# Kernel tuning notes

Measured on AMD Instinct MI355X. Metric: run time of the kernel, lower is better.

Reference implementation:

```python
import jax, jax.numpy as jnp
import numpy as np

THETA = 10000.0


def apply_rope(x, token_position, theta=THETA):
    # x: [B, H, S, d_k] with interleaved even/odd pairs; token_position: [B, S]
    B, H, S, d_k = x.shape
    inv_freq = 1.0 / theta ** (jnp.arange(0, d_k, 2, dtype=jnp.float32) / d_k)  # [d_k/2]
    angles = token_position.astype(jnp.float32)[:, :, None] * inv_freq[None, None, :]  # [B,S,d_k/2]
    cos = jnp.cos(angles)[:, None, :, :]  # [B,1,S,d_k/2]
    sin = jnp.sin(angles)[:, None, :, :]
    xp = x.reshape(B, H, S, d_k // 2, 2)
    x_even, x_odd = xp[..., 0], xp[..., 1]
    rot_even = x_even * cos - x_odd * sin
    rot_odd = x_even * sin + x_odd * cos
    return jnp.stack([rot_even, rot_odd], axis=-1).reshape(B, H, S, d_k)


def setup_inputs() -> dict:
    key = jax.random.key(0)
    ks = jax.random.split(key, 6)
    B, S, D = 2, 2048, 2048
    x = jax.random.normal(ks[0], (B, S, D), dtype=jnp.float32)
    token_position = jnp.sort(jax.random.randint(ks[1], (B, S), 0, 2048), axis=-1).astype(jnp.int32)
    scale = 0.02
    WQ = jax.random.normal(ks[2], (D, D), dtype=jnp.float32) * scale
    WK = jax.random.normal(ks[3], (D, D), dtype=jnp.float32) * scale
    WV = jax.random.normal(ks[4], (D, D), dtype=jnp.float32) * scale
    WO = jax.random.normal(ks[5], (D, D), dtype=jnp.float32) * scale
    return {"x": x, "token_position": token_position, "WQ": WQ, "WK": WK, "WV": WV, "WO": WO}


def reference(x, token_position, WQ, WK, WV, WO):
    B, S, D = x.shape
    H = 16
    d_k = D // H

    def proj(W):
        return jnp.matmul(x, W).reshape(B, S, H, d_k).transpose(0, 2, 1, 3)  # [B,H,S,d_k]

    Q = apply_rope(proj(WQ), token_position)
    K = apply_rope(proj(WK), token_position)
    V = proj(WV)

    score = jnp.einsum('bhqd,bhkd->bhqk', Q, K) / jnp.sqrt(jnp.float32(d_k))
    causal = jnp.triu(jnp.full((S, S), -jnp.inf, dtype=jnp.float32), k=1)
    score = score + causal
    attn = jax.nn.softmax(score, axis=-1)  # stable max-sub softmax, same math
    out = jnp.einsum('bhqk,bhkd->bhqd', attn, V)
    out = out.transpose(0, 2, 1, 3).reshape(B, S, D)
    return jnp.matmul(out, WO)
```

## Files before the change

### kernel.cpp

```cpp
#include <hip/hip_runtime.h>
#include <hip/hip_bf16.h>
#include <cstdint>
#include <cstddef>

typedef unsigned short u16;
typedef __attribute__((ext_vector_type(4))) unsigned short u16x4;
typedef __attribute__((ext_vector_type(8))) unsigned short u16x8;
typedef __attribute__((ext_vector_type(8))) __bf16 bf16x8;
typedef __attribute__((ext_vector_type(4))) float f32x4;

#define MFMA16(a, b, c) __builtin_amdgcn_mfma_f32_16x16x32_bf16((a), (b), (c), 0, 0, 0)

__device__ __forceinline__ u16 f2bf(float f) {
  uint32_t u = __builtin_bit_cast(uint32_t, f);
  u += 0x7FFFu + ((u >> 16) & 1u);
  return (u16)(u >> 16);
}
__device__ __forceinline__ float bf2f(u16 h) {
  return __builtin_bit_cast(float, (uint32_t)h << 16);
}

typedef const __attribute__((address_space(1))) void gv_t;
typedef __attribute__((address_space(3))) void lv_t;
__device__ __forceinline__ void gload16(const void* g, void* l) {
  __builtin_amdgcn_global_load_lds((gv_t*)g, (lv_t*)l, 16, 0, 0);
}

__global__ void prep(const float* __restrict__ x, const float* __restrict__ w0,
                     const float* __restrict__ w1, const float* __restrict__ w2,
                     const float* __restrict__ w3, u16* __restrict__ xb,
                     u16* __restrict__ wtbase) {
  const int z = blockIdx.z;
  const int bx = blockIdx.x, by = blockIdx.y;
  const int tx = threadIdx.x, ty = threadIdx.y;
  if (z >= 4) {
    const int i = ((z - 4) * 4096 + by * 64 + bx) * 256 + ty * 32 + tx;
    float4 v = ((const float4*)x)[i];
    u16x4 o;
    o[0] = f2bf(v.x); o[1] = f2bf(v.y); o[2] = f2bf(v.z); o[3] = f2bf(v.w);
    ((u16x4*)xb)[i] = o;
    return;
  }
  __shared__ float tile[32][33];
  const float* in = (z == 0) ? w0 : (z == 1) ? w1 : (z == 2) ? w2 : w3;
  u16* out = wtbase + (size_t)z * 4194304;
#pragma unroll
  for (int i = 0; i < 32; i += 8)
    tile[ty + i][tx] = in[(size_t)(by * 32 + ty + i) * 2048 + bx * 32 + tx];
  __syncthreads();
#pragma unroll
  for (int i = 0; i < 32; i += 8)
    out[(size_t)(bx * 32 + ty + i) * 2048 + by * 32 + tx] = f2bf(tile[tx][ty + i]);
}

template <int MODE>
__global__ __launch_bounds__(512, 1) void gemm8(const u16* __restrict__ A,
                                                const u16* __restrict__ Bt,
                                                void* __restrict__ Cv,
                                                const int* __restrict__ pos, int nbn) {
  constexpr int K = 2048;
  __shared__ __align__(16) u16 lds[73728];
  const int tid = threadIdx.x, lane = tid & 63;
  const int lo16 = lane & 15, hi = lane >> 4;
  const int wid = tid >> 6;
  const int wr = wid >> 1, wc = wid & 1;

  const int xcd = (int)blockIdx.x & 7;
  const int idx = (int)blockIdx.x >> 3;
  const int cpx = nbn >> 3;
  const int bn = (xcd * cpx + idx % cpx) * 128;
  const int bm = (idx / cpx) * 256;

  const int srow = tid >> 3;
  const int scol = ((tid & 7) ^ (srow & 7)) * 8;
  const u16* Arow = A + (size_t)(bm + srow) * K + scol;
  const u16* Brow = Bt + (size_t)(bn + srow) * K + scol;
  char* dstbase = (char*)lds + tid * 16;

#define STG_A(qb_, t_, r_) \
  gload16(Arow + (size_t)(r_) * 64 * K + (t_) * 64, dstbase + (qb_) * 49152 + (r_) * 8192)
#define STG_B(qb_, t_, r_) \
  gload16(Brow + (size_t)(r_) * 64 * K + (t_) * 64, dstbase + (qb_) * 49152 + 32768 + (r_) * 8192)

  f32x4 acc[4][4];
  const f32x4 z4 = {0.f, 0.f, 0.f, 0.f};
#pragma unroll
  for (int m = 0; m < 4; ++m)
#pragma unroll
    for (int n = 0; n < 4; ++n) acc[m][n] = z4;

  const int xork = lo16 & 7;
  const int aRow = (wr * 64 + lo16) * 128;
  const int bRow = 32768 + (wc * 64 + lo16) * 128;
  const int x0 = ((hi ^ xork)) << 4;
  const int x1 = (((4 + hi) ^ xork)) << 4;

  STG_A(0, 0, 0); STG_A(0, 0, 1); STG_A(0, 0, 2); STG_A(0, 0, 3);
  STG_B(0, 0, 0); STG_B(0, 0, 1);
  STG_A(1, 1, 0); STG_A(1, 1, 1); STG_A(1, 1, 2); STG_A(1, 1, 3);
  STG_B(1, 1, 0); STG_B(1, 1, 1);

  int q = 0;
  for (int t = 0; t < 32; ++t) {
    if (t < 31) {
      asm volatile("s_waitcnt vmcnt(6)" ::: "memory");
    } else {
      asm volatile("s_waitcnt vmcnt(0)" ::: "memory");
    }
    __builtin_amdgcn_s_barrier();
    __builtin_amdgcn_sched_barrier(0);
    const char* Aq = (const char*)lds + q * 49152;
    const int q2 = (q == 0) ? 2 : q - 1;

    bf16x8 a0[4], b0[4], a1[4], b1[4];
#pragma unroll
    for (int m = 0; m < 4; ++m) a0[m] = *(const bf16x8*)(Aq + aRow + m * 2048 + x0);
#pragma unroll
    for (int n = 0; n < 4; ++n) b0[n] = *(const bf16x8*)(Aq + bRow + n * 2048 + x0);
#pragma unroll
    for (int m = 0; m < 4; ++m) a1[m] = *(const bf16x8*)(Aq + aRow + m * 2048 + x1);
#pragma unroll
    for (int n = 0; n < 4; ++n) b1[n] = *(const bf16x8*)(Aq + bRow + n * 2048 + x1);

    if (t < 30) {
      STG_A(q2, t + 2, 0); STG_A(q2, t + 2, 1); STG_A(q2, t + 2, 2); STG_A(q2, t + 2, 3);
      STG_B(q2, t + 2, 0); STG_B(q2, t + 2, 1);
    }

    __builtin_amdgcn_s_setprio(1);
#pragma unroll
    for (int m = 0; m < 4; ++m)
#pragma unroll
      for (int n = 0; n < 4; ++n) acc[m][n] = MFMA16(a0[m], b0[n], acc[m][n]);
#pragma unroll
    for (int m = 0; m < 4; ++m)
#pragma unroll
      for (int n = 0; n < 4; ++n) acc[m][n] = MFMA16(a1[m], b1[n], acc[m][n]);
    __builtin_amdgcn_s_setprio(0);
    q = (q == 2) ? 0 : q + 1;
  }
#undef STG_A
#undef STG_B

  if constexpr (MODE == 2) {
    const int sect = bn >> 11;
    u16* Cq = (u16*)Cv + (size_t)sect * 8388608;
    const int cb = (bn & 2047) + wc * 64;
    if (sect < 2) {
      const float qsc = (sect == 0) ? 0.12751743f : 1.0f;
      float freq[4];
#pragma unroll
      for (int n = 0; n < 4; ++n) {
        const int c = cb + n * 16 + lo16;
        freq[n] = exp2f((float)((c & 127) >> 1) * -0.2076205059304601f);
      }
      const float sg = (lo16 & 1) ? 1.f : -1.f;
#pragma unroll
      for (int m = 0; m < 4; ++m) {
        const int row = bm + wr * 64 + m * 16 + hi * 4;
#pragma unroll
        for (int r = 0; r < 4; ++r) {
          const float p = (float)pos[row + r];
#pragma unroll
          for (int n = 0; n < 4; ++n) {
            const float ang = p * freq[n];
            const float sn = __sinf(ang);
            const float cs = __cosf(ang);
            const float v = acc[m][n][r];
            const float pv = __shfl_xor(v, 1);
            Cq[(size_t)(row + r) * 2048 + cb + n * 16 + lo16] =
                f2bf((v * cs + sg * pv * sn) * qsc);
          }
        }
      }
    } else {
      __syncthreads();
#pragma unroll
      for (int m = 0; m < 4; ++m) {
#pragma unroll
        for (int n = 0; n < 4; ++n) {
          const int d = wc * 64 + n * 16 + lo16;
          const int tokb = wr * 64 + m * 16 + hi * 4;
#pragma unroll
          for (int r = 0; r < 4; ++r)
            lds[d * 260 + tokb + r] = f2bf(acc[m][n][r]);
        }
      }
      __syncthreads();
      const int b = bm >> 11, hh = (bn & 2047) >> 7;
      u16* vt = Cq + ((size_t)((b * 16 + hh) * 128)) * 2048 + (bm & 2047);
#pragma unroll
      for (int j = 0; j < 4; ++j) {
        const int d = (tid >> 4) + j * 32;
        const int t0 = (tid & 15) * 16;
        const u16* src = lds + d * 260 + t0;
        u16* dst = vt + (size_t)d * 2048 + t0;
#pragma unroll
        for (int w = 0; w < 4; ++w)
          *(u16x4*)(dst + w * 4) = *(const u16x4*)(src + w * 4);
      }
    }
  } else {
    float* C = (float*)Cv;
    const int cb = bn + wc * 64;
#pragma unroll
    for (int m = 0; m < 4; ++m)
#pragma unroll
      for (int n = 0; n < 4; ++n)
#pragma unroll
        for (int r = 0; r < 4; ++r)
          C[(size_t)(bm + wr * 64 + m * 16 + hi * 4 + r) * 2048 + cb + n * 16 + lo16] =
              acc[m][n][r];
  }
}

__device__ __forceinline__ void sm_write(f32x4* accS, float* m_r, float* l_r,
                                         f32x4* accO, char* Pw, int lane) {
  float lm[4];
#pragma unroll
  for (int j = 0; j < 4; ++j)
    lm[j] = fmaxf(fmaxf(accS[0][j], accS[1][j]), fmaxf(accS[2][j], accS[3][j]));
  const bool ok = (lm[0] <= m_r[0] + 11.5f) && (lm[1] <= m_r[1] + 11.5f) &&
                  (lm[2] <= m_r[2] + 11.5f) && (lm[3] <= m_r[3] + 11.5f);
  if (!__all(ok)) {
#pragma unroll
    for (int j = 0; j < 4; ++j) {
      float mx = lm[j];
#pragma unroll
      for (int off = 1; off < 16; off <<= 1) mx = fmaxf(mx, __shfl_xor(mx, off));
      const float mn = fmaxf(m_r[j], mx);
      const float sc = exp2f(m_r[j] - mn);
      m_r[j] = mn;
      l_r[j] *= sc;
#pragma unroll
      for (int db = 0; db < 8; ++db) accO[db][j] *= sc;
    }
  }
#pragma unroll
  for (int j = 0; j < 4; ++j) {
    float s = 0.f;
    const int ql = (lane >> 4) * 4 + j;
#pragma unroll
    for (int nb = 0; nb < 4; ++nb) {
      const float p = exp2f(accS[nb][j] - m_r[j]);
      s += p;
      const int col = nb * 16 + (lane & 15);
      const int byteoff = ql * 128 + ((((col >> 3) ^ (ql & 7))) << 4) + (col & 7) * 2;
      *(u16*)(Pw + byteoff) = (u16)(__builtin_bit_cast(uint32_t, p) >> 16);
    }
    l_r[j] += s;
  }
}

__global__ __launch_bounds__(256, 2) void flash_attn9(const u16* __restrict__ Qb,
                                                      const u16* __restrict__ Kb,
                                                      const u16* __restrict__ VT,
                                                      u16* __restrict__ Ob) {
  constexpr int S = 2048, HD = 2048;
  const int g = (int)blockIdx.x;
  const int xcd = g & 7, slot = g >> 3;
  const int bh = xcd * 4 + (slot & 3);
  const int pairid = slot >> 2;
  const int b = bh >> 4, h = bh & 15;
  const int tid = threadIdx.x, lane = tid & 63, wid = tid >> 6;
  const int qtA = 31 - pairid, qtB = pairid;
  const int q0a = qtA * 64, q0b = qtB * 64;

  __shared__ u16 Ks[2][64 * 128];
  __shared__ u16 Vs[2][128 * 64];
  __shared__ u16 Ps[4][2][16 * 64];

  const size_t base = (size_t)b * S * HD + (size_t)h * 128;
  const u16* Qp = Qb + base;
  const u16* Kp = Kb + base;
  const u16* VTp = VT + (size_t)bh * 128 * S;
  u16* Op = Ob + base;

  const f32x4 z4 = {0.f, 0.f, 0.f, 0.f};
  const int kKv = (lane >> 4);
  const int kC16 = (lane & 15);
  const int vD = (lane >> 3);
  const int vC16 = (lane & 7);

#define STAGE(pb, kv0_)                                                                   \
  {                                                                                       \
    _Pragma("unroll") for (int c = 0; c < 4; ++c) {                                       \
      const int ch = wid * 4 + c;                                                         \
      {                                                                                   \
        const int kv = ch * 4 + kKv;                                                      \
        const int c16 = kC16 ^ (kv & 7);                                                  \
        gload16(Kp + (size_t)((kv0_) + kv) * HD + c16 * 8, (char*)Ks[pb] + ch * 1024);    \
      }                                                                                   \
      {                                                                                   \
        const int d = ch * 8 + vD;                                                        \
        const int c16 = vC16 ^ (d & 7);                                                   \
        gload16(VTp + (size_t)d * S + (kv0_) + c16 * 8, (char*)Vs[pb] + ch * 1024);       \
      }                                                                                   \
    }                                                                                     \
  }

  bf16x8 qfA[4], qfB[4];
  {
    const int kc = (lane >> 4) * 8;
    const int qrA = q0a + wid * 16 + (lane & 15);
    const int qrB = q0b + wid * 16 + (lane & 15);
#pragma unroll
    for (int kb = 0; kb < 4; ++kb) {
      qfA[kb] = *(const bf16x8*)(Qp + (size_t)qrA * HD + kb * 32 + kc);
      qfB[kb] = *(const bf16x8*)(Qp + (size_t)qrB * HD + kb * 32 + kc);
    }
  }

  f32x4 accOA[8], accOB[8];
#pragma unroll
  for (int d = 0; d < 8; ++d) { accOA[d] = z4; accOB[d] = z4; }
  float mA[4] = {-INFINITY, -INFINITY, -INFINITY, -INFINITY};
  float lA[4] = {0.f, 0.f, 0.f, 0.f};
  float mB[4] = {-INFINITY, -INFINITY, -INFINITY, -INFINITY};
  float lB[4] = {0.f, 0.f, 0.f, 0.f};

  const int qrow0A = q0a + wid * 16 + (lane >> 4) * 4;
  const int qrow0B = q0b + wid * 16 + (lane >> 4) * 4;
  char* Pw0 = (char*)&Ps[wid][0][0];
  char* Pw1 = (char*)&Ps[wid][1][0];

  STAGE(0, 0);

  int t = 0;
  for (; t <= qtB; ++t) {
    const int cur = t & 1;
    const int kv0 = t * 64;
    STAGE(cur ^ 1, kv0 + 64);
    asm volatile("s_waitcnt vmcnt(8)" ::: "memory");
    __builtin_amdgcn_s_barrier();
    __builtin_amdgcn_sched_barrier(0);

    const char* Ksc = (const char*)Ks[cur];
    const char* Vsc = (const char*)Vs[cur];

    f32x4 sA[4], sB[4];
#pragma unroll
    for (int nb = 0; nb < 4; ++nb) { sA[nb] = z4; sB[nb] = z4; }
    __builtin_amdgcn_s_setprio(1);
#pragma unroll
    for (int nb = 0; nb < 4; ++nb) {
      const int kv = nb * 16 + (lane & 15);
#pragma unroll
      for (int kb = 0; kb < 4; ++kb) {
        const int c16 = (kb * 4 + (lane >> 4)) ^ (kv & 7);
        bf16x8 kf = *(const bf16x8*)(Ksc + kv * 256 + c16 * 16);
        sA[nb] = MFMA16(qfA[kb], kf, sA[nb]);
        sB[nb] = MFMA16(qfB[kb], kf, sB[nb]);
      }
    }
    __builtin_amdgcn_s_setprio(0);

    if (t == qtB) {
#pragma unroll
      for (int nb = 0; nb < 4; ++nb) {
        const int kv = kv0 + nb * 16 + (lane & 15);
#pragma unroll
        for (int j = 0; j < 4; ++j)
          if (kv > qrow0B + j) sB[nb][j] = -INFINITY;
      }
    }

    sm_write(sA, mA, lA, accOA, Pw0, lane);
    sm_write(sB, mB, lB, accOB, Pw1, lane);

#pragma unroll
    for (int kb2 = 0; kb2 < 2; ++kb2) {
      const int ql = lane & 15;
      const int c16a = (kb2 * 4 + (lane >> 4)) ^ (ql & 7);
      bf16x8 paA = *(const bf16x8*)(Pw0 + ql * 128 + c16a * 16);
      bf16x8 paB = *(const bf16x8*)(Pw1 + ql * 128 + c16a * 16);
      __builtin_amdgcn_s_setprio(1);
#pragma unroll
      for (int db = 0; db < 8; ++db) {
        const int d = db * 16 + (lane & 15);
        const int c16 = (kb2 * 4 + (lane >> 4)) ^ (d & 7);
        bf16x8 vf = *(const bf16x8*)(Vsc + d * 128 + c16 * 16);
        accOA[db] = MFMA16(paA, vf, accOA[db]);
        accOB[db] = MFMA16(paB, vf, accOB[db]);
      }
      __builtin_amdgcn_s_setprio(0);
    }
    __builtin_amdgcn_sched_barrier(0);
    __builtin_amdgcn_s_barrier();
  }

  for (; t <= qtA; ++t) {
    const int cur = t & 1;
    const int kv0 = t * 64;
    if (t < qtA) {
      STAGE(cur ^ 1, kv0 + 64);
      asm volatile("s_waitcnt vmcnt(8)" ::: "memory");
    } else {
      asm volatile("s_waitcnt vmcnt(0)" ::: "memory");
    }
    __builtin_amdgcn_s_barrier();
    __builtin_amdgcn_sched_barrier(0);

    const char* Ksc = (const char*)Ks[cur];
    const char* Vsc = (const char*)Vs[cur];

    f32x4 sA[4];
#pragma unroll
    for (int nb = 0; nb < 4; ++nb) sA[nb] = z4;
    __builtin_amdgcn_s_setprio(1);
#pragma unroll
    for (int nb = 0; nb < 4; ++nb) {
      const int kv = nb * 16 + (lane & 15);
#pragma unroll
      for (int kb = 0; kb < 4; ++kb) {
        const int c16 = (kb * 4 + (lane >> 4)) ^ (kv & 7);
        bf16x8 kf = *(const bf16x8*)(Ksc + kv * 256 + c16 * 16);
        sA[nb] = MFMA16(qfA[kb], kf, sA[nb]);
      }
    }
    __builtin_amdgcn_s_setprio(0);

    if (t == qtA) {
#pragma unroll
      for (int nb = 0; nb < 4; ++nb) {
        const int kv = kv0 + nb * 16 + (lane & 15);
#pragma unroll
        for (int j = 0; j < 4; ++j)
          if (kv > qrow0A + j) sA[nb][j] = -INFINITY;
      }
    }

    sm_write(sA, mA, lA, accOA, Pw0, lane);

#pragma unroll
    for (int kb2 = 0; kb2 < 2; ++kb2) {
      const int ql = lane & 15;
      const int c16a = (kb2 * 4 + (lane >> 4)) ^ (ql & 7);
      bf16x8 paA = *(const bf16x8*)(Pw0 + ql * 128 + c16a * 16);
      __builtin_amdgcn_s_setprio(1);
#pragma unroll
      for (int db = 0; db < 8; ++db) {
        const int d = db * 16 + (lane & 15);
        const int c16 = (kb2 * 4 + (lane >> 4)) ^ (d & 7);
        bf16x8 vf = *(const bf16x8*)(Vsc + d * 128 + c16 * 16);
        accOA[db] = MFMA16(paA, vf, accOA[db]);
      }
      __builtin_amdgcn_s_setprio(0);
    }
    __builtin_amdgcn_sched_barrier(0);
    __builtin_amdgcn_s_barrier();
  }
#undef STAGE

  float invA[4], invB[4];
#pragma unroll
  for (int j = 0; j < 4; ++j) {
    float la = lA[j], lb = lB[j];
#pragma unroll
    for (int off = 1; off < 16; off <<= 1) {
      la += __shfl_xor(la, off);
      lb += __shfl_xor(lb, off);
    }
    invA[j] = 1.f / la;
    invB[j] = 1.f / lb;
  }
#pragma unroll
  for (int db = 0; db < 8; ++db)
#pragma unroll
    for (int j = 0; j < 4; ++j) {
      const int rowA = qrow0A + j;
      const int rowB = qrow0B + j;
      Op[(size_t)rowA * HD + db * 16 + (lane & 15)] = f2bf(accOA[db][j] * invA[j]);
      Op[(size_t)rowB * HD + db * 16 + (lane & 15)] = f2bf(accOB[db][j] * invB[j]);
    }
}

extern "C" void kernel_launch(void* const* d_in, const int* in_sizes, int n_in,
                              void* d_out, int out_size, void* d_ws, size_t ws_size,
                              hipStream_t stream) {
  const float* x  = (const float*)d_in[0];
  const int*   tp = (const int*)d_in[1];
  const float* WQ = (const float*)d_in[2];
  const float* WK = (const float*)d_in[3];
  const float* WV = (const float*)d_in[4];
  const float* WO = (const float*)d_in[5];

  const size_t MB = 1024 * 1024;
  if (ws_size < 112 * MB) return;
  char* ws = (char*)d_ws;
  u16* xb  = (u16*)(ws + 0 * MB);
  u16* wqt = (u16*)(ws + 16 * MB);
  u16* wot = (u16*)(ws + 40 * MB);
  u16* Qb  = (u16*)(ws + 48 * MB);
  u16* Kb  = (u16*)(ws + 64 * MB);
  u16* VTb = (u16*)(ws + 80 * MB);
  u16* Obf = (u16*)(ws + 96 * MB);

  {
    dim3 g(64, 64, 6), blk(32, 8);
    prep<<<g, blk, 0, stream>>>(x, WQ, WK, WV, WO, xb, wqt);
  }
  gemm8<2><<<768, 512, 0, stream>>>(xb, wqt, (void*)Qb, tp, 48);

  flash_attn9<<<512, 256, 0, stream>>>(Qb, Kb, VTb, Obf);

  gemm8<1><<<256, 512, 0, stream>>>(Obf, wot, d_out, nullptr, 16);
}
```

Before: 236.8 us.

## Halve GEMM N-tile to 64 and switch to double-buffered LDS pipeline

The GEMM tile width in N drops from 128 to 64, so twice as many blocks are launched and each block needs less LDS (80KB instead of 144KB). The launch bound is raised to allow several blocks per CU. The triple-buffered prefetch-two-ahead pipeline becomes a double buffer that issues the next stage before waiting, with an extra barrier at the end of each iteration. The aim is more occupancy and a better-filled grid for the projection GEMMs. The cost is lower arithmetic intensity per block, more global traffic for the A tile, and an added sync per k-step.

```diff
diff --git a/kernel.cpp b/kernel.cpp
--- a/kernel.cpp
+++ b/kernel.cpp
@@ -54,12 +54,12 @@
 }
 
 template <int MODE>
-__global__ __launch_bounds__(512, 1) void gemm8(const u16* __restrict__ A,
+__global__ __launch_bounds__(512, 4) void gemm8(const u16* __restrict__ A,
                                                 const u16* __restrict__ Bt,
                                                 void* __restrict__ Cv,
                                                 const int* __restrict__ pos, int nbn) {
   constexpr int K = 2048;
-  __shared__ __align__(16) u16 lds[73728];
+  __shared__ __align__(16) u16 lds[40960];
   const int tid = threadIdx.x, lane = tid & 63;
   const int lo16 = lane & 15, hi = lane >> 4;
   const int wid = tid >> 6;
@@ -68,7 +68,7 @@
   const int xcd = (int)blockIdx.x & 7;
   const int idx = (int)blockIdx.x >> 3;
   const int cpx = nbn >> 3;
-  const int bn = (xcd * cpx + idx % cpx) * 128;
+  const int bn = (xcd * cpx + idx % cpx) * 64;
   const int bm = (idx / cpx) * 256;
 
   const int srow = tid >> 3;
@@ -78,79 +78,74 @@
   char* dstbase = (char*)lds + tid * 16;
 
 #define STG_A(qb_, t_, r_) \
-  gload16(Arow + (size_t)(r_) * 64 * K + (t_) * 64, dstbase + (qb_) * 49152 + (r_) * 8192)
-#define STG_B(qb_, t_, r_) \
-  gload16(Brow + (size_t)(r_) * 64 * K + (t_) * 64, dstbase + (qb_) * 49152 + 32768 + (r_) * 8192)
-
-  f32x4 acc[4][4];
+  gload16(Arow + (size_t)(r_) * 64 * K + (t_) * 64, dstbase + (qb_) * 40960 + (r_) * 8192)
+#define STG_B(qb_, t_) \
+  gload16(Brow + (t_) * 64, dstbase + (qb_) * 40960 + 32768)
+#define STAGE(qb_, t_) \
+  { STG_A(qb_, t_, 0); STG_A(qb_, t_, 1); STG_A(qb_, t_, 2); STG_A(qb_, t_, 3); STG_B(qb_, t_); }
+
+  f32x4 acc[4][2];
   const f32x4 z4 = {0.f, 0.f, 0.f, 0.f};
 #pragma unroll
   for (int m = 0; m < 4; ++m)
 #pragma unroll
-    for (int n = 0; n < 4; ++n) acc[m][n] = z4;
+    for (int n = 0; n < 2; ++n) acc[m][n] = z4;
 
   const int xork = lo16 & 7;
   const int aRow = (wr * 64 + lo16) * 128;
-  const int bRow = 32768 + (wc * 64 + lo16) * 128;
+  const int bRow = 32768 + (wc * 32 + lo16) * 128;
   const int x0 = ((hi ^ xork)) << 4;
   const int x1 = (((4 + hi) ^ xork)) << 4;
 
-  STG_A(0, 0, 0); STG_A(0, 0, 1); STG_A(0, 0, 2); STG_A(0, 0, 3);
-  STG_B(0, 0, 0); STG_B(0, 0, 1);
-  STG_A(1, 1, 0); STG_A(1, 1, 1); STG_A(1, 1, 2); STG_A(1, 1, 3);
-  STG_B(1, 1, 0); STG_B(1, 1, 1);
-
-  int q = 0;
+  STAGE(0, 0);
+
   for (int t = 0; t < 32; ++t) {
     if (t < 31) {
-      asm volatile("s_waitcnt vmcnt(6)" ::: "memory");
+      STAGE((t + 1) & 1, t + 1);
+      asm volatile("s_waitcnt vmcnt(5)" ::: "memory");
     } else {
       asm volatile("s_waitcnt vmcnt(0)" ::: "memory");
     }
     __builtin_amdgcn_s_barrier();
     __builtin_amdgcn_sched_barrier(0);
-    const char* Aq = (const char*)lds + q * 49152;
-    const int q2 = (q == 0) ? 2 : q - 1;
-
-    bf16x8 a0[4], b0[4], a1[4], b1[4];
+    const char* Aq = (const char*)lds + (t & 1) * 40960;
+
+    bf16x8 a0[4], a1[4], b0[2], b1[2];
 #pragma unroll
     for (int m = 0; m < 4; ++m) a0[m] = *(const bf16x8*)(Aq + aRow + m * 2048 + x0);
 #pragma unroll
-    for (int n = 0; n < 4; ++n) b0[n] = *(const bf16x8*)(Aq + bRow + n * 2048 + x0);
+    for (int n = 0; n < 2; ++n) b0[n] = *(const bf16x8*)(Aq + bRow + n * 2048 + x0);
 #pragma unroll
     for (int m = 0; m < 4; ++m) a1[m] = *(const bf16x8*)(Aq + aRow + m * 2048 + x1);
 #pragma unroll
-    for (int n = 0; n < 4; ++n) b1[n] = *(const bf16x8*)(Aq + bRow + n * 2048 + x1);
-
-    if (t < 30) {
-      STG_A(q2, t + 2, 0); STG_A(q2, t + 2, 1); STG_A(q2, t + 2, 2); STG_A(q2, t + 2, 3);
-      STG_B(q2, t + 2, 0); STG_B(q2, t + 2, 1);
-    }
+    for (int n = 0; n < 2; ++n) b1[n] = *(const bf16x8*)(Aq + bRow + n * 2048 + x1);
 
     __builtin_amdgcn_s_setprio(1);
 #pragma unroll
     for (int m = 0; m < 4; ++m)
 #pragma unroll
-      for (int n = 0; n < 4; ++n) acc[m][n] = MFMA16(a0[m], b0[n], acc[m][n]);
+      for (int n = 0; n < 2; ++n) acc[m][n] = MFMA16(a0[m], b0[n], acc[m][n]);
 #pragma unroll
     for (int m = 0; m < 4; ++m)
 #pragma unroll
-      for (int n = 0; n < 4; ++n) acc[m][n] = MFMA16(a1[m], b1[n], acc[m][n]);
+      for (int n = 0; n < 2; ++n) acc[m][n] = MFMA16(a1[m], b1[n], acc[m][n]);
     __builtin_amdgcn_s_setprio(0);
-    q = (q == 2) ? 0 : q + 1;
+    __builtin_amdgcn_sched_barrier(0);
+    __builtin_amdgcn_s_barrier();
   }
 #undef STG_A
 #undef STG_B
+#undef STAGE
 
   if constexpr (MODE == 2) {
     const int sect = bn >> 11;
     u16* Cq = (u16*)Cv + (size_t)sect * 8388608;
-    const int cb = (bn & 2047) + wc * 64;
+    const int cb = (bn & 2047) + wc * 32;
     if (sect < 2) {
       const float qsc = (sect == 0) ? 0.12751743f : 1.0f;
-      float freq[4];
-#pragma unroll
-      for (int n = 0; n < 4; ++n) {
+      float freq[2];
+#pragma unroll
+      for (int n = 0; n < 2; ++n) {
         const int c = cb + n * 16 + lo16;
         freq[n] = exp2f((float)((c & 127) >> 1) * -0.2076205059304601f);
       }
@@ -162,7 +157,7 @@
         for (int r = 0; r < 4; ++r) {
           const float p = (float)pos[row + r];
 #pragma unroll
-          for (int n = 0; n < 4; ++n) {
+          for (int n = 0; n < 2; ++n) {
             const float ang = p * freq[n];
             const float sn = __sinf(ang);
             const float cs = __cosf(ang);
@@ -178,23 +173,25 @@
 #pragma unroll
       for (int m = 0; m < 4; ++m) {
 #pragma unroll
-        for (int n = 0; n < 4; ++n) {
-          const int d = wc * 64 + n * 16 + lo16;
+        for (int n = 0; n < 2; ++n) {
+          const int dl = wc * 32 + n * 16 + lo16;
           const int tokb = wr * 64 + m * 16 + hi * 4;
 #pragma unroll
           for (int r = 0; r < 4; ++r)
-            lds[d * 260 + tokb + r] = f2bf(acc[m][n][r]);
+            lds[dl * 260 + tokb + r] = f2bf(acc[m][n][r]);
         }
       }
       __syncthreads();
-      const int b = bm >> 11, hh = (bn & 2047) >> 7;
-      u16* vt = Cq + ((size_t)((b * 16 + hh) * 128)) * 2048 + (bm & 2047);
-#pragma unroll
-      for (int j = 0; j < 4; ++j) {
-        const int d = (tid >> 4) + j * 32;
+      const int b = bm >> 11;
+      const int col = bn & 2047;
+      const int hh = col >> 7, d0 = col & 127;
+      u16* vt = Cq + ((size_t)((b * 16 + hh) * 128 + d0)) * 2048 + (bm & 2047);
+#pragma unroll
+      for (int j = 0; j < 2; ++j) {
+        const int dl = (tid >> 4) + j * 32;
         const int t0 = (tid & 15) * 16;
-        const u16* src = lds + d * 260 + t0;
-        u16* dst = vt + (size_t)d * 2048 + t0;
+        const u16* src = lds + dl * 260 + t0;
+        u16* dst = vt + (size_t)dl * 2048 + t0;
 #pragma unroll
         for (int w = 0; w < 4; ++w)
           *(u16x4*)(dst + w * 4) = *(const u16x4*)(src + w * 4);
@@ -202,11 +199,11 @@
     }
   } else {
     float* C = (float*)Cv;
-    const int cb = bn + wc * 64;
+    const int cb = bn + wc * 32;
 #pragma unroll
     for (int m = 0; m < 4; ++m)
 #pragma unroll
-      for (int n = 0; n < 4; ++n)
+      for (int n = 0; n < 2; ++n)
 #pragma unroll
         for (int r = 0; r < 4; ++r)
           C[(size_t)(bm + wr * 64 + m * 16 + hi * 4 + r) * 2048 + cb + n * 16 + lo16] =
@@ -500,9 +497,9 @@
     dim3 g(64, 64, 6), blk(32, 8);
     prep<<<g, blk, 0, stream>>>(x, WQ, WK, WV, WO, xb, wqt);
   }
-  gemm8<2><<<768, 512, 0, stream>>>(xb, wqt, (void*)Qb, tp, 48);
+  gemm8<2><<<1536, 512, 0, stream>>>(xb, wqt, (void*)Qb, tp, 96);
 
   flash_attn9<<<512, 256, 0, stream>>>(Qb, Kb, VTb, Obf);
 
-  gemm8<1><<<256, 512, 0, stream>>>(Obf, wot, d_out, nullptr, 16);
-}
+  gemm8<1><<<512, 512, 0, stream>>>(Obf, wot, d_out, nullptr, 32);
+}
```

Result: slower. 243.7 us (+2.9%).
